# Kernel optimization log

Measured on AMD Instinct MI355X. Metric: run time of the kernel, lower is better.

## Reference

```python
import jax, jax.numpy as jnp
import numpy as np

N_EXPERTS = 20
DIM = 32
EPS = 1e-12  # F.normalize eps


def setup_inputs() -> dict:
    key = jax.random.key(0)
    k_x, k_pos, k_w1, k_b1, k_w0, k_b0 = jax.random.split(key, 6)
    B = 131072
    bound = 1.0 / np.sqrt(DIM)  # torch Linear default init range
    return {
        "x": jax.random.normal(k_x, (B, DIM), dtype=jnp.float32),
        "W1": jax.random.uniform(k_w1, (N_EXPERTS, DIM, DIM), jnp.float32, -bound, bound),
        "b1": jax.random.uniform(k_b1, (N_EXPERTS, DIM), jnp.float32, -bound, bound),
        "W0": jax.random.uniform(k_w0, (N_EXPERTS, DIM, DIM), jnp.float32, -bound, bound),
        "b0": jax.random.uniform(k_b0, (N_EXPERTS, DIM), jnp.float32, -bound, bound),
        "pos": jax.random.randint(k_pos, (B,), 0, N_EXPERTS, dtype=jnp.int64),
    }


def reference(x, W1, b1, W0, b0, pos):
    # Gather per-sample expert weights (routing): [B, DIM, DIM] / [B, DIM]
    W1g, b1g = W1[pos], b1[pos]
    W0g, b0g = W0[pos], b0[pos]
    # fc1: y = x @ W1^T + b1 (torch Linear convention, W is [out, in])
    h = jnp.einsum("bi,boi->bo", x, W1g) + b1g
    # fc0
    out = jnp.einsum("bi,boi->bo", h, W0g) + b0g
    # F.normalize(dim=-1): x / max(||x||_2, eps)
    norm = jnp.sqrt(jnp.sum(out * out, axis=-1, keepdims=True))
    return out / jnp.maximum(norm, EPS)
```

## Files before the change

kernel.cpp:

```cpp
#include <hip/hip_runtime.h>
#include <stdint.h>

#define N_EXPERTS 20
#define DIM 32
#define SPB 256
#define MAIN_T 512
#define MROW 40
#define XROW 40
#define MAX_TILES 48

using frag_ab = __attribute__((ext_vector_type(8))) short;
using frag_cd = __attribute__((ext_vector_type(4))) float;

static __device__ __forceinline__ short f2bf(float f) {
    union { float f; uint32_t u; } v; v.f = f;
    uint32_t u = v.u;
    return (short)(uint16_t)((u + 0x7FFFu + ((u >> 16) & 1u)) >> 16);
}

__global__ __launch_bounds__(256) void k_prep(
    const float* __restrict__ W1, const float* __restrict__ b1,
    const float* __restrict__ W0, const float* __restrict__ b0,
    unsigned short* __restrict__ Mbf, float* __restrict__ cvec)
{
    __shared__ float s1[1024], s0[1024];
    int e = blockIdx.x, t = threadIdx.x;
    const float* w1 = W1 + e * 1024;
    const float* w0 = W0 + e * 1024;
    for (int i = t; i < 1024; i += 256) { s1[i] = w1[i]; s0[i] = w0[i]; }
    __syncthreads();
    for (int idx = t; idx < 1024; idx += 256) {
        int o = idx >> 5, i = idx & 31;
        float s = 0.f;
        #pragma unroll
        for (int k = 0; k < 32; k++) s += s0[o*32 + k] * s1[k*32 + i];
        Mbf[e*1024 + o*32 + i] = (unsigned short)f2bf(s);
    }
    if (t < DIM) {
        float s = b0[e*32 + t];
        #pragma unroll
        for (int k = 0; k < 32; k++) s += s0[t*32 + k] * b1[e*32 + k];
        cvec[e*32 + t] = s;
    }
}

__global__ __launch_bounds__(MAIN_T, 4) void k_moe(
    const float* __restrict__ x, const int* __restrict__ pos,
    const unsigned short* __restrict__ Mbf, const float* __restrict__ cvec,
    float* __restrict__ out, int B)
{
    __shared__ unsigned short Ms[N_EXPERTS * 32 * MROW];
    __shared__ unsigned short Xs[SPB * XROW];
    __shared__ float cs[N_EXPERTS * 32];
    __shared__ int hist[N_EXPERTS];
    __shared__ int lstart[N_EXPERTS + 1];
    __shared__ int cursor[N_EXPERTS];
    __shared__ int lidx[SPB];
    __shared__ int tileE[MAX_TILES], tileB[MAX_TILES];
    __shared__ int ntiles;

    int t = threadIdx.x;
    int base = blockIdx.x * SPB;
    int S = min(SPB, B - base);
    if (S <= 0) return;

    if (t < N_EXPERTS) hist[t] = 0;
    int my_e = -1;
    if (t < S) my_e = pos[base + t];
    __syncthreads();
    if (t < S) atomicAdd(&hist[my_e], 1);

    {
        const uint32_t* msrc = (const uint32_t*)Mbf;
        uint32_t* mdst = (uint32_t*)Ms;
        for (int d = t; d < N_EXPERTS * 512; d += MAIN_T) {
            int e = d >> 9, rem = d & 511;
            int n = rem >> 4, c = rem & 15;
            mdst[e * (32 * MROW / 2) + n * (MROW / 2) + c] = msrc[d];
        }
        for (int i = t; i < N_EXPERTS * 32; i += MAIN_T) cs[i] = cvec[i];
    }
    for (int d = t; d < 2 * S; d += MAIN_T) {
        int s = d >> 1, half = d & 1;
        const float* xr = x + (size_t)(base + s) * 32 + half * 16;
        float4 a = *(const float4*)(xr);
        float4 b = *(const float4*)(xr + 4);
        float4 c = *(const float4*)(xr + 8);
        float4 e4 = *(const float4*)(xr + 12);
        frag_ab v0, v1;
        v0[0] = f2bf(a.x); v0[1] = f2bf(a.y); v0[2] = f2bf(a.z); v0[3] = f2bf(a.w);
        v0[4] = f2bf(b.x); v0[5] = f2bf(b.y); v0[6] = f2bf(b.z); v0[7] = f2bf(b.w);
        v1[0] = f2bf(c.x); v1[1] = f2bf(c.y); v1[2] = f2bf(c.z); v1[3] = f2bf(c.w);
        v1[4] = f2bf(e4.x); v1[5] = f2bf(e4.y); v1[6] = f2bf(e4.z); v1[7] = f2bf(e4.w);
        unsigned short* xd = (unsigned short*)Xs + s * XROW + half * 16;
        *(frag_ab*)(xd)     = v0;
        *(frag_ab*)(xd + 8) = v1;
    }
    __syncthreads();

    int lane = t & 63, wave = t >> 6;

    if (wave == 0) {
        int e = lane;
        int h = (e < N_EXPERTS) ? hist[e] : 0;
        int s = h;
        #pragma unroll
        for (int d = 1; d < 32; d <<= 1) { int v = __shfl_up(s, d); if (lane >= d) s += v; }
        int pre = s - h;
        int ntl = (h + 15) >> 4;
        int ts = ntl;
        #pragma unroll
        for (int d = 1; d < 32; d <<= 1) { int v = __shfl_up(ts, d); if (lane >= d) ts += v; }
        int tpre = ts - ntl;
        if (e < N_EXPERTS) {
            lstart[e] = pre; cursor[e] = pre;
            for (int k = 0; k < ntl; k++) { tileE[tpre + k] = e; tileB[tpre + k] = pre + 16 * k; }
            if (e == N_EXPERTS - 1) { lstart[N_EXPERTS] = pre + h; ntiles = tpre + ntl; }
        }
    }
    __syncthreads();

    if (t < S) {
        int slot = atomicAdd(&cursor[my_e], 1);
        lidx[slot] = t;
    }
    __syncthreads();

    int nt = ntiles;
    int n = lane & 15, q = lane >> 4;

    for (int ti = wave; ti < nt; ti += (MAIN_T / 64)) {
        int e = tileE[ti], tb = tileB[ti];
        int bend = lstart[e + 1];

        int slot = min(tb + n, bend - 1);
        int l = lidx[slot];

        frag_ab af = *(const frag_ab*)((const unsigned short*)Xs + l * XROW + q * 8);

        const unsigned short* mrow = Ms + e * 32 * MROW;
        frag_ab bf0 = *(const frag_ab*)(mrow + n * MROW + q * 8);
        frag_ab bf1 = *(const frag_ab*)(mrow + (n + 16) * MROW + q * 8);
        float c0 = cs[e * 32 + n];
        float c1 = cs[e * 32 + 16 + n];

        frag_cd z = {0.f, 0.f, 0.f, 0.f};
        frag_cd d0 = __builtin_amdgcn_mfma_f32_16x16x32_bf16(af, bf0, z, 0, 0, 0);
        frag_cd d1 = __builtin_amdgcn_mfma_f32_16x16x32_bf16(af, bf1, z, 0, 0, 0);

        #pragma unroll
        for (int r = 0; r < 4; r++) {
            int os = tb + q * 4 + r;
            float v0 = d0[r] + c0;
            float v1 = d1[r] + c1;
            float ss = v0 * v0 + v1 * v1;
            ss += __shfl_xor(ss, 1);
            ss += __shfl_xor(ss, 2);
            ss += __shfl_xor(ss, 4);
            ss += __shfl_xor(ss, 8);
            float sc = rsqrtf(fmaxf(ss, 1e-24f));
            if (os < bend) {
                int lo = lidx[os];
                float* op = out + (size_t)(base + lo) * 32;
                op[n]      = v0 * sc;
                op[16 + n] = v1 * sc;
            }
        }
    }
}

extern "C" void kernel_launch(void* const* d_in, const int* in_sizes, int n_in,
                              void* d_out, int out_size, void* d_ws, size_t ws_size,
                              hipStream_t stream) {
    const float* x  = (const float*)d_in[0];
    const float* W1 = (const float*)d_in[1];
    const float* b1 = (const float*)d_in[2];
    const float* W0 = (const float*)d_in[3];
    const float* b0 = (const float*)d_in[4];
    const int*  pos = (const int*)d_in[5];
    float* out = (float*)d_out;
    int B = in_sizes[0] / DIM;

    char* ws = (char*)d_ws;
    unsigned short* Mbf = (unsigned short*)ws;
    float* cvec = (float*)(ws + (size_t)N_EXPERTS * 1024 * 2);

    k_prep<<<N_EXPERTS, 256, 0, stream>>>(W1, b1, W0, b0, Mbf, cvec);
    int nblk = (B + SPB - 1) / SPB;
    k_moe<<<nblk, MAIN_T, 0, stream>>>(x, pos, Mbf, cvec, out, B);
}
```

Before: 86.78 us.

## Read expert matrices from global/L2 instead of staging in LDS, shrink blocks

Stops copying all 20 fused expert matrices and bias vectors into shared memory in every block; each wave now loads its B fragments and bias directly from global memory, relying on L2/L1 caching. The block size is halved to 128 samples and 256 threads. The x loads are issued before the histogram barrier so they overlap with it, and output stores become nontemporal. This removes a large per-block LDS fill and improves occupancy, at the cost of uncached-fragment global loads inside the tile loop.

```diff
diff --git a/kernel.cpp b/kernel.cpp
--- a/kernel.cpp
+++ b/kernel.cpp
@@ -3,11 +3,10 @@
 
 #define N_EXPERTS 20
 #define DIM 32
-#define SPB 256
-#define MAIN_T 512
-#define MROW 40
+#define SPB 128
+#define MAIN_T 256
 #define XROW 40
-#define MAX_TILES 48
+#define MAX_TILES 32
 
 using frag_ab = __attribute__((ext_vector_type(8))) short;
 using frag_cd = __attribute__((ext_vector_type(4))) float;
@@ -25,9 +24,8 @@
 {
     __shared__ float s1[1024], s0[1024];
     int e = blockIdx.x, t = threadIdx.x;
-    const float* w1 = W1 + e * 1024;
-    const float* w0 = W0 + e * 1024;
-    for (int i = t; i < 1024; i += 256) { s1[i] = w1[i]; s0[i] = w0[i]; }
+    ((float4*)s1)[t] = ((const float4*)(W1 + e * 1024))[t];
+    ((float4*)s0)[t] = ((const float4*)(W0 + e * 1024))[t];
     __syncthreads();
     for (int idx = t; idx < 1024; idx += 256) {
         int o = idx >> 5, i = idx & 31;
@@ -49,9 +47,7 @@
     const unsigned short* __restrict__ Mbf, const float* __restrict__ cvec,
     float* __restrict__ out, int B)
 {
-    __shared__ unsigned short Ms[N_EXPERTS * 32 * MROW];
     __shared__ unsigned short Xs[SPB * XROW];
-    __shared__ float cs[N_EXPERTS * 32];
     __shared__ int hist[N_EXPERTS];
     __shared__ int lstart[N_EXPERTS + 1];
     __shared__ int cursor[N_EXPERTS];
@@ -64,35 +60,30 @@
     int S = min(SPB, B - base);
     if (S <= 0) return;
 
+    int my_e = (t < S) ? pos[base + t] : -1;
+
+    int s_row = t >> 1, half = t & 1;
+    bool xs_act = (t < 2 * S);
+    float4 a, b, c, d;
+    if (xs_act) {
+        const float* xr = x + (size_t)(base + s_row) * 32 + half * 16;
+        a = *(const float4*)(xr);
+        b = *(const float4*)(xr + 4);
+        c = *(const float4*)(xr + 8);
+        d = *(const float4*)(xr + 12);
+    }
+
     if (t < N_EXPERTS) hist[t] = 0;
-    int my_e = -1;
-    if (t < S) my_e = pos[base + t];
     __syncthreads();
     if (t < S) atomicAdd(&hist[my_e], 1);
 
-    {
-        const uint32_t* msrc = (const uint32_t*)Mbf;
-        uint32_t* mdst = (uint32_t*)Ms;
-        for (int d = t; d < N_EXPERTS * 512; d += MAIN_T) {
-            int e = d >> 9, rem = d & 511;
-            int n = rem >> 4, c = rem & 15;
-            mdst[e * (32 * MROW / 2) + n * (MROW / 2) + c] = msrc[d];
-        }
-        for (int i = t; i < N_EXPERTS * 32; i += MAIN_T) cs[i] = cvec[i];
-    }
-    for (int d = t; d < 2 * S; d += MAIN_T) {
-        int s = d >> 1, half = d & 1;
-        const float* xr = x + (size_t)(base + s) * 32 + half * 16;
-        float4 a = *(const float4*)(xr);
-        float4 b = *(const float4*)(xr + 4);
-        float4 c = *(const float4*)(xr + 8);
-        float4 e4 = *(const float4*)(xr + 12);
+    if (xs_act) {
         frag_ab v0, v1;
         v0[0] = f2bf(a.x); v0[1] = f2bf(a.y); v0[2] = f2bf(a.z); v0[3] = f2bf(a.w);
         v0[4] = f2bf(b.x); v0[5] = f2bf(b.y); v0[6] = f2bf(b.z); v0[7] = f2bf(b.w);
         v1[0] = f2bf(c.x); v1[1] = f2bf(c.y); v1[2] = f2bf(c.z); v1[3] = f2bf(c.w);
-        v1[4] = f2bf(e4.x); v1[5] = f2bf(e4.y); v1[6] = f2bf(e4.z); v1[7] = f2bf(e4.w);
-        unsigned short* xd = (unsigned short*)Xs + s * XROW + half * 16;
+        v1[4] = f2bf(d.x); v1[5] = f2bf(d.y); v1[6] = f2bf(d.z); v1[7] = f2bf(d.w);
+        unsigned short* xd = (unsigned short*)Xs + s_row * XROW + half * 16;
         *(frag_ab*)(xd)     = v0;
         *(frag_ab*)(xd + 8) = v1;
     }
@@ -105,12 +96,12 @@
         int h = (e < N_EXPERTS) ? hist[e] : 0;
         int s = h;
         #pragma unroll
-        for (int d = 1; d < 32; d <<= 1) { int v = __shfl_up(s, d); if (lane >= d) s += v; }
+        for (int dd = 1; dd < 32; dd <<= 1) { int v = __shfl_up(s, dd); if (lane >= dd) s += v; }
         int pre = s - h;
         int ntl = (h + 15) >> 4;
         int ts = ntl;
         #pragma unroll
-        for (int d = 1; d < 32; d <<= 1) { int v = __shfl_up(ts, d); if (lane >= d) ts += v; }
+        for (int dd = 1; dd < 32; dd <<= 1) { int v = __shfl_up(ts, dd); if (lane >= dd) ts += v; }
         int tpre = ts - ntl;
         if (e < N_EXPERTS) {
             lstart[e] = pre; cursor[e] = pre;
@@ -138,11 +129,11 @@
 
         frag_ab af = *(const frag_ab*)((const unsigned short*)Xs + l * XROW + q * 8);
 
-        const unsigned short* mrow = Ms + e * 32 * MROW;
-        frag_ab bf0 = *(const frag_ab*)(mrow + n * MROW + q * 8);
-        frag_ab bf1 = *(const frag_ab*)(mrow + (n + 16) * MROW + q * 8);
-        float c0 = cs[e * 32 + n];
-        float c1 = cs[e * 32 + 16 + n];
+        const unsigned short* me = Mbf + e * 1024;
+        frag_ab bf0 = *(const frag_ab*)(me + n * 32 + q * 8);
+        frag_ab bf1 = *(const frag_ab*)(me + (n + 16) * 32 + q * 8);
+        float c0 = cvec[e * 32 + n];
+        float c1 = cvec[e * 32 + 16 + n];
 
         frag_cd z = {0.f, 0.f, 0.f, 0.f};
         frag_cd d0 = __builtin_amdgcn_mfma_f32_16x16x32_bf16(af, bf0, z, 0, 0, 0);
@@ -162,8 +153,8 @@
             if (os < bend) {
                 int lo = lidx[os];
                 float* op = out + (size_t)(base + lo) * 32;
-                op[n]      = v0 * sc;
-                op[16 + n] = v1 * sc;
+                __builtin_nontemporal_store(v0 * sc, op + n);
+                __builtin_nontemporal_store(v1 * sc, op + 16 + n);
             }
         }
     }
```

Result: no change. 85.60 us (-1.4%).
